# Optimization experiments

Hardware: AMD Instinct MI355X
Metric: run time of the kernel (lower is better)

The kernel has to match this reference:

```python
import jax, jax.numpy as jnp
import numpy as np

B, T, F, H = 1024, 512, 32, 64
EPS = 1e-3  # keras BatchNormalization default epsilon


def lstm_layer(x, Wx, Uh, b):
    """Keras LSTM with activation=relu, recurrent_activation=sigmoid.
    x: [B,T,Fin]; Wx: [Fin,4H]; Uh: [H,4H]; b: [4H]. Gate order i,f,c,o."""
    xz = jnp.einsum('btf,fg->btg', x, Wx) + b  # precompute input projection
    h0 = jnp.zeros((x.shape[0], Uh.shape[0]), x.dtype)

    def step(carry, xz_t):
        h, c = carry
        z = xz_t + h @ Uh
        i, f, g, o = jnp.split(z, 4, axis=-1)
        i = jax.nn.sigmoid(i)
        f = jax.nn.sigmoid(f)
        o = jax.nn.sigmoid(o)
        c = f * c + i * jax.nn.relu(g)
        h = o * jax.nn.relu(c)
        return (h, c), h

    _, hs = jax.lax.scan(step, (h0, h0), jnp.swapaxes(xz, 0, 1))  # [T,B,H]
    return jnp.swapaxes(hs, 0, 1)  # [B,T,H]


def batchnorm(x, gamma, beta, mean, var):
    # inference-mode BN over last axis (keras default axis=-1, training=False)
    return (x - mean) * (gamma * jax.lax.rsqrt(var + EPS)) + beta


def attention(x, W, ht):
    # score = (X @ W) @ h_t -> [B,T]; softmax over time; c_t = X^T @ alpha
    score = jnp.einsum('btd,de,e->bt', x, W, ht[:, 0])
    alpha = jax.nn.softmax(score, axis=1)
    return jnp.einsum('btd,bt->bd', x, alpha)  # [B,H]


def setup_inputs() -> dict:
    key = jax.random.key(0)
    ks = jax.random.split(key, 32)
    d = {'x': jax.random.normal(ks[0], (B, T, F), jnp.float32)}
    fins = [F, H, H]
    for l in range(3):
        fin = fins[l]
        i = l + 1
        d[f'w{i}'] = jax.random.normal(ks[1 + 9 * l], (fin, 4 * H), jnp.float32) * (1.0 / np.sqrt(fin))
        d[f'u{i}'] = jax.random.normal(ks[2 + 9 * l], (H, 4 * H), jnp.float32) * (1.0 / np.sqrt(H))
        d[f'bi{i}'] = jnp.zeros((4 * H,), jnp.float32)
        d[f'gamma{i}'] = jnp.ones((H,), jnp.float32)
        d[f'beta{i}'] = jnp.zeros((H,), jnp.float32)
        d[f'mean{i}'] = jax.random.normal(ks[3 + 9 * l], (H,), jnp.float32) * 0.1
        d[f'var{i}'] = jnp.ones((H,), jnp.float32) + jax.random.uniform(ks[4 + 9 * l], (H,), jnp.float32) * 0.1
        d[f'attw{i}'] = jax.random.truncated_normal(ks[5 + 9 * l], -2, 2, (H, H), jnp.float32) * 0.5
        d[f'attv{i}'] = jax.random.truncated_normal(ks[6 + 9 * l], -2, 2, (H, 1), jnp.float32) * 0.5
    d['dw'] = jax.random.normal(ks[30], (3 * H, 1), jnp.float32) * (1.0 / np.sqrt(3 * H))
    d['db'] = jnp.zeros((1,), jnp.float32)
    return d


def reference(x, w1, u1, bi1, gamma1, beta1, mean1, var1, attw1, attv1,
              w2, u2, bi2, gamma2, beta2, mean2, var2, attw2, attv2,
              w3, u3, bi3, gamma3, beta3, mean3, var3, attw3, attv3,
              dw, db):
    h = lstm_layer(x, w1, u1, bi1)
    h = batchnorm(h, gamma1, beta1, mean1, var1)
    a1 = attention(h, attw1, attv1)
    h = lstm_layer(h, w2, u2, bi2)
    h = batchnorm(h, gamma2, beta2, mean2, var2)
    a2 = attention(h, attw2, attv2)
    h = lstm_layer(h, w3, u3, bi3)
    h = batchnorm(h, gamma3, beta3, mean3, var3)
    a3 = attention(h, attw3, attv3)
    feat = jnp.concatenate([a1, a2, a3], axis=1)  # [B, 3H]
    return feat @ dw + db  # [B, 1]
```

## Files before the change

### kernel.cpp

```cpp
#include <hip/hip_runtime.h>
#include <math.h>

#define BB 1024
#define TT 512
#define FF 32
#define HH 64
#define GG 256
#define TC 64
#define NCHUNK (TT/TC)
#define MB 16
#define NBLK 64
#define HSTR 72
#define EPSBN 1e-3f

typedef __attribute__((ext_vector_type(8))) short bf16x8;
typedef __attribute__((ext_vector_type(4))) float f32x4;
typedef __attribute__((ext_vector_type(4))) int   i32x4;
typedef unsigned short ushort_t;

__global__ void fold1_kernel(const float* __restrict__ gamma, const float* __restrict__ beta,
                             const float* __restrict__ mean, const float* __restrict__ var,
                             const float* __restrict__ attw, const float* __restrict__ attv,
                             float* __restrict__ s_out, float* __restrict__ ab_out,
                             float* __restrict__ wv_out) {
    int d = threadIdx.x;
    float s = gamma[d] * rsqrtf(var[d] + EPSBN);
    float ab = beta[d] - mean[d] * s;
    float wvr = 0.f;
    for (int e = 0; e < HH; ++e) wvr += attw[d * HH + e] * attv[e];
    s_out[d] = s;
    ab_out[d] = ab;
    wv_out[d] = s * wvr;
}

__global__ void fold2_kernel(const float* __restrict__ W, const float* __restrict__ b,
                             const float* __restrict__ s_prev, const float* __restrict__ ab_prev,
                             float* __restrict__ Wp, float* __restrict__ bp) {
    int g = threadIdx.x;
    float bacc = b[g];
    for (int d = 0; d < HH; ++d) {
        float w = W[d * GG + g];
        bacc += ab_prev[d] * w;
        Wp[d * GG + g] = s_prev[d] * w;
    }
    bp[g] = bacc;
}

__global__ void init_kernel(float* st_h, float* st_c, float* st_acc, float* st_m, float* st_d) {
    int i = blockIdx.x * blockDim.x + threadIdx.x;
    int n = 3 * BB * HH;
    if (i < n) { st_h[i] = 0.f; st_c[i] = 0.f; st_acc[i] = 0.f; }
    if (i < 3 * BB) { st_m[i] = -3.0e38f; st_d[i] = 0.f; }
}

__device__ __forceinline__ f32x4 ld4(const float* p) { return *reinterpret_cast<const f32x4*>(p); }
__device__ __forceinline__ void st4(float* p, f32x4 v) { *reinterpret_cast<f32x4*>(p) = v; }
__device__ __forceinline__ bf16x8 ldbf(const ushort_t* p) { return *reinterpret_cast<const bf16x8*>(p); }
__device__ __forceinline__ int cvtpk(float a, float b) {
    int r; asm("v_cvt_pk_bf16_f32 %0, %1, %2" : "=v"(r) : "v"(a), "v"(b)); return r;
}
__device__ __forceinline__ float sigm(float x) { return __fdividef(1.f, 1.f + __expf(-x)); }
#define MFMA(a, b, c) c = __builtin_amdgcn_mfma_f32_16x16x32_bf16(a, b, c, 0, 0, 0)

__global__ void prep_frags(const float* __restrict__ M, int KT, ushort_t* __restrict__ outF) {
    int idx = blockIdx.x * 256 + threadIdx.x;
    int tot = 16 * KT * 512;
    if (idx >= tot) return;
    int e = idx & 7, l = (idx >> 3) & 63, f = idx >> 9;
    int kt = f % KT, gw = f / KT;
    int g = gw & 3, w = gw >> 2;
    int r = l & 15, q = l >> 4;
    int k = 32 * kt + 8 * q + e;
    int col = 64 * g + 16 * w + r;
    float v = M[(size_t)k * GG + col];
    int hb = cvtpk(v, v) & 0xffff;
    float hf = __int_as_float(hb << 16);
    float lo = v - hf;
    int lb = cvtpk(lo, lo) & 0xffff;
    outF[(size_t)(f * 2 + 0) * 512 + l * 8 + e] = (ushort_t)hb;
    outF[(size_t)(f * 2 + 1) * 512 + l * 8 + e] = (ushort_t)lb;
}

__global__ void prep_planes(const float* __restrict__ in, ushort_t* __restrict__ hi,
                            ushort_t* __restrict__ lo, int n4) {
    int i = blockIdx.x * 256 + threadIdx.x;
    if (i >= n4) return;
    f32x4 v = reinterpret_cast<const f32x4*>(in)[i];
    int p0 = cvtpk(v[0], v[1]), p1 = cvtpk(v[2], v[3]);
    float a0 = v[0] - __int_as_float(p0 << 16);
    float a1 = v[1] - __int_as_float(p0 & 0xffff0000);
    float a2 = v[2] - __int_as_float(p1 << 16);
    float a3 = v[3] - __int_as_float(p1 & 0xffff0000);
    int q0 = cvtpk(a0, a1), q1 = cvtpk(a2, a3);
    reinterpret_cast<int2*>(hi)[i] = make_int2(p0, p1);
    reinterpret_cast<int2*>(lo)[i] = make_int2(q0, q1);
}

struct RecFArgs {
    const ushort_t* xhi[3]; const ushort_t* xlo[3]; long sB[3]; long sT[3]; int K[3];
    const ushort_t* UF[3]; const ushort_t* WF[3]; const float* bias[3];
    ushort_t* Hhi[3]; ushort_t* Hlo[3];
    float* st_h[3]; float* st_c[3]; float* st_acc[3];
    float* st_m[3]; float* st_d[3];
    const float* wv[3]; const float* abv[3]; const float* sbn[3];
    float* a_out[3];
    int last[3]; int first[3];
};

template<int KT>
__device__ __forceinline__ void rec_body(const RecFArgs& A, const int seg, const int b0,
                                         ushort_t* hbf, float* scoreP) {
    const int tid = threadIdx.x;
    const int w = tid >> 6;
    const int l = tid & 63;
    const int r = l & 15;
    const int q = l >> 4;
    const int cw = w << 4;
    const int grow = b0 + r;

    const bf16x8* UF = reinterpret_cast<const bf16x8*>(A.UF[seg]);
    const bf16x8* WF = reinterpret_cast<const bf16x8*>(A.WF[seg]);
#define LDU(g,kt,p_) UF[(((((w<<2)+(g))*2+(kt))*2)+(p_))*64 + l]
#define LDW(g,kt,p_) WF[(((((w<<2)+(g))*KT+(kt))*2)+(p_))*64 + l]
    bf16x8 uh00=LDU(0,0,0), uh01=LDU(0,1,0), uh10=LDU(1,0,0), uh11=LDU(1,1,0),
           uh20=LDU(2,0,0), uh21=LDU(2,1,0), uh30=LDU(3,0,0), uh31=LDU(3,1,0);
    bf16x8 ul00=LDU(0,0,1), ul01=LDU(0,1,1), ul10=LDU(1,0,1), ul11=LDU(1,1,1),
           ul20=LDU(2,0,1), ul21=LDU(2,1,1), ul30=LDU(3,0,1), ul31=LDU(3,1,1);
    bf16x8 wh00=LDW(0,0,0), wh10=LDW(1,0,0), wh20=LDW(2,0,0), wh30=LDW(3,0,0);
    bf16x8 wl00=LDW(0,0,1), wl10=LDW(1,0,1), wl20=LDW(2,0,1), wl30=LDW(3,0,1);
    bf16x8 wh01{}, wh11{}, wh21{}, wh31{}, wl01{}, wl11{}, wl21{}, wl31{};
    if constexpr (KT == 2) {
        wh01=LDW(0,1,0); wh11=LDW(1,1,0); wh21=LDW(2,1,0); wh31=LDW(3,1,0);
        wl01=LDW(0,1,1); wl11=LDW(1,1,1); wl21=LDW(2,1,1); wl31=LDW(3,1,1);
    }

    f32x4 bias40 = ld4(A.bias[seg] +   0 + cw + 4 * q);
    f32x4 bias41 = ld4(A.bias[seg] +  64 + cw + 4 * q);
    f32x4 bias42 = ld4(A.bias[seg] + 128 + cw + 4 * q);
    f32x4 bias43 = ld4(A.bias[seg] + 192 + cw + 4 * q);
    f32x4 wv4 = ld4(A.wv[seg] + cw + 4 * q);

    f32x4 c4   = ld4(A.st_c[seg]   + (size_t)grow * HH + cw + 4 * q);
    f32x4 h4   = ld4(A.st_h[seg]   + (size_t)grow * HH + cw + 4 * q);
    f32x4 acc4 = ld4(A.st_acc[seg] + (size_t)grow * HH + cw + 4 * q);
    float m_b = A.st_m[seg][grow];
    float d_b = A.st_d[seg][grow];

    int2 hs_hi, hs_lo;
    auto publish = [&](int slot, f32x4 hv) {
        int p0 = cvtpk(hv[0], hv[1]), p1 = cvtpk(hv[2], hv[3]);
        float a0 = hv[0] - __int_as_float(p0 << 16);
        float a1 = hv[1] - __int_as_float(p0 & 0xffff0000);
        float a2 = hv[2] - __int_as_float(p1 << 16);
        float a3 = hv[3] - __int_as_float(p1 & 0xffff0000);
        int q0 = cvtpk(a0, a1), q1 = cvtpk(a2, a3);
        hs_hi = make_int2(p0, p1); hs_lo = make_int2(q0, q1);
        *reinterpret_cast<int2*>(hbf + ((slot * 2 + 0) * 16 + r) * HSTR + cw + 4 * q) = hs_hi;
        *reinterpret_cast<int2*>(hbf + ((slot * 2 + 1) * 16 + r) * HSTR + cw + 4 * q) = hs_lo;
        float part = hv[0] * wv4[0];
        part = fmaf(hv[1], wv4[1], part);
        part = fmaf(hv[2], wv4[2], part);
        part = fmaf(hv[3], wv4[3], part);
        part += __shfl_xor(part, 16);
        part += __shfl_xor(part, 32);
        if (q == 0) scoreP[(slot * 4 + w) * 16 + r] = part;
    };

    publish(0, h4);

    const ushort_t* xhib = A.xhi[seg] + (size_t)grow * A.sB[seg];
    const ushort_t* xlob = A.xlo[seg] + (size_t)grow * A.sB[seg];
    const long sT = A.sT[seg];

    bf16x8 xh0 = ldbf(xhib + 8 * q), xl0 = ldbf(xlob + 8 * q);
    bf16x8 xh1{}, xl1{};
    if constexpr (KT == 2) { xh1 = ldbf(xhib + 32 + 8 * q); xl1 = ldbf(xlob + 32 + 8 * q); }
    __syncthreads();

    const bool first = A.first[seg] != 0;
    ushort_t* Hhi = A.Hhi[seg];
    ushort_t* Hlo = A.Hlo[seg];

#pragma unroll 2
    for (int t = 0; t < TC; ++t) {
        const int pr = t & 1;
        if (Hhi && t > 0) {
            size_t ho = (size_t)grow * (TC * HH) + (size_t)(t - 1) * HH + cw + 4 * q;
            *reinterpret_cast<int2*>(Hhi + ho) = hs_hi;
            *reinterpret_cast<int2*>(Hlo + ho) = hs_lo;
        }
        float sc = scoreP[(pr * 4 + q) * 16 + r];
        sc += __shfl_xor(sc, 16);
        sc += __shfl_xor(sc, 32);
        if (!(first && t == 0)) {
            float mn = fmaxf(m_b, sc);
            float corr = __expf(m_b - mn);
            float p = __expf(sc - mn);
            d_b = d_b * corr + p;
            acc4 = acc4 * corr + p * h4;
            m_b = mn;
        }
        const int tn = (t + 1 < TC) ? t + 1 : TC - 1;
        const ushort_t* xph = xhib + (size_t)tn * sT + 8 * q;
        const ushort_t* xpl = xlob + (size_t)tn * sT + 8 * q;
        bf16x8 nh0 = ldbf(xph), nl0 = ldbf(xpl), nh1{}, nl1{};
        if constexpr (KT == 2) { nh1 = ldbf(xph + 32); nl1 = ldbf(xpl + 32); }

        const ushort_t* hbh = hbf + (pr * 2 + 0) * 16 * HSTR + r * HSTR;
        const ushort_t* hbl = hbf + (pr * 2 + 1) * 16 * HSTR + r * HSTR;
        bf16x8 bh0 = ldbf(hbh + 8 * q);
        bf16x8 bh1 = ldbf(hbh + 32 + 8 * q);
        bf16x8 bl0 = ldbf(hbl + 8 * q);
        bf16x8 bl1 = ldbf(hbl + 32 + 8 * q);

        f32x4 C0 = bias40;
        MFMA(wh00, xh0, C0); MFMA(wh00, xl0, C0); MFMA(wl00, xh0, C0);
        if constexpr (KT == 2) { MFMA(wh01, xh1, C0); MFMA(wh01, xl1, C0); MFMA(wl01, xh1, C0); }
        MFMA(uh00, bh0, C0); MFMA(uh00, bl0, C0); MFMA(ul00, bh0, C0);
        MFMA(uh01, bh1, C0); MFMA(uh01, bl1, C0); MFMA(ul01, bh1, C0);
        f32x4 C1 = bias41;
        MFMA(wh10, xh0, C1); MFMA(wh10, xl0, C1); MFMA(wl10, xh0, C1);
        if constexpr (KT == 2) { MFMA(wh11, xh1, C1); MFMA(wh11, xl1, C1); MFMA(wl11, xh1, C1); }
        MFMA(uh10, bh0, C1); MFMA(uh10, bl0, C1); MFMA(ul10, bh0, C1);
        MFMA(uh11, bh1, C1); MFMA(uh11, bl1, C1); MFMA(ul11, bh1, C1);
        f32x4 C2 = bias42;
        MFMA(wh20, xh0, C2); MFMA(wh20, xl0, C2); MFMA(wl20, xh0, C2);
        if constexpr (KT == 2) { MFMA(wh21, xh1, C2); MFMA(wh21, xl1, C2); MFMA(wl21, xh1, C2); }
        MFMA(uh20, bh0, C2); MFMA(uh20, bl0, C2); MFMA(ul20, bh0, C2);
        MFMA(uh21, bh1, C2); MFMA(uh21, bl1, C2); MFMA(ul21, bh1, C2);
        f32x4 C3 = bias43;
        MFMA(wh30, xh0, C3); MFMA(wh30, xl0, C3); MFMA(wl30, xh0, C3);
        if constexpr (KT == 2) { MFMA(wh31, xh1, C3); MFMA(wh31, xl1, C3); MFMA(wl31, xh1, C3); }
        MFMA(uh30, bh0, C3); MFMA(uh30, bl0, C3); MFMA(ul30, bh0, C3);
        MFMA(uh31, bh1, C3); MFMA(uh31, bl1, C3); MFMA(ul31, bh1, C3);

#pragma unroll
        for (int i = 0; i < 4; ++i) {
            float zi = sigm(C0[i]);
            float zf = sigm(C1[i]);
            float zg = fmaxf(C2[i], 0.f);
            float zo = sigm(C3[i]);
            c4[i] = fmaf(zf, c4[i], zi * zg);
            h4[i] = zo * fmaxf(c4[i], 0.f);
        }
        publish(pr ^ 1, h4);

        xh0 = nh0; xl0 = nl0;
        if constexpr (KT == 2) { xh1 = nh1; xl1 = nl1; }
        __syncthreads();
    }

    if (Hhi) {
        size_t ho = (size_t)grow * (TC * HH) + (size_t)(TC - 1) * HH + cw + 4 * q;
        *reinterpret_cast<int2*>(Hhi + ho) = hs_hi;
        *reinterpret_cast<int2*>(Hlo + ho) = hs_lo;
    }
    if (A.last[seg]) {
        float sc = scoreP[(0 * 4 + q) * 16 + r];
        sc += __shfl_xor(sc, 16);
        sc += __shfl_xor(sc, 32);
        float mn = fmaxf(m_b, sc);
        float corr = __expf(m_b - mn);
        float p = __expf(sc - mn);
        d_b = d_b * corr + p;
        acc4 = acc4 * corr + p * h4;
        m_b = mn;
        f32x4 sb = ld4(A.sbn[seg] + cw + 4 * q);
        f32x4 ab = ld4(A.abv[seg] + cw + 4 * q);
        f32x4 res;
#pragma unroll
        for (int i = 0; i < 4; ++i)
            res[i] = sb[i] * __fdividef(acc4[i], d_b) + ab[i];
        st4(A.a_out[seg] + (size_t)grow * HH + cw + 4 * q, res);
    }
    st4(A.st_c[seg]   + (size_t)grow * HH + cw + 4 * q, c4);
    st4(A.st_h[seg]   + (size_t)grow * HH + cw + 4 * q, h4);
    st4(A.st_acc[seg] + (size_t)grow * HH + cw + 4 * q, acc4);
    if (w == 0 && q == 0) { A.st_m[seg][grow] = m_b; A.st_d[seg][grow] = d_b; }
#undef LDU
#undef LDW
}

__global__ __launch_bounds__(256, 2) void rec_mfma(RecFArgs A) {
    __shared__ ushort_t hbf[2 * 2 * 16 * HSTR];
    __shared__ float scoreP[2 * 4 * 16];
    const int seg = blockIdx.x >> 6;
    const int b0 = (blockIdx.x & (NBLK - 1)) << 4;
    if (A.K[seg] == 32) rec_body<1>(A, seg, b0, hbf, scoreP);
    else                rec_body<2>(A, seg, b0, hbf, scoreP);
}

__global__ void final_kernel(const float* __restrict__ a, const float* __restrict__ dw,
                             const float* __restrict__ db, float* __restrict__ out) {
    int b = blockIdx.x * blockDim.x + threadIdx.x;
    if (b >= BB) return;
    float acc = db[0];
    for (int l = 0; l < 3; ++l)
        for (int j = 0; j < HH; ++j)
            acc += a[(l * BB + b) * HH + j] * dw[l * HH + j];
    out[b] = acc;
}

extern "C" void kernel_launch(void* const* d_in, const int* in_sizes, int n_in,
                              void* d_out, int out_size, void* d_ws, size_t ws_size,
                              hipStream_t stream) {
    (void)in_sizes; (void)n_in; (void)out_size; (void)ws_size;
    const float* x = (const float*)d_in[0];
    const float* w[3]    = {(const float*)d_in[1],  (const float*)d_in[10], (const float*)d_in[19]};
    const float* uu[3]   = {(const float*)d_in[2],  (const float*)d_in[11], (const float*)d_in[20]};
    const float* bi[3]   = {(const float*)d_in[3],  (const float*)d_in[12], (const float*)d_in[21]};
    const float* gam[3]  = {(const float*)d_in[4],  (const float*)d_in[13], (const float*)d_in[22]};
    const float* bet[3]  = {(const float*)d_in[5],  (const float*)d_in[14], (const float*)d_in[23]};
    const float* mea[3]  = {(const float*)d_in[6],  (const float*)d_in[15], (const float*)d_in[24]};
    const float* var[3]  = {(const float*)d_in[7],  (const float*)d_in[16], (const float*)d_in[25]};
    const float* atw[3]  = {(const float*)d_in[8],  (const float*)d_in[17], (const float*)d_in[26]};
    const float* atv[3]  = {(const float*)d_in[9],  (const float*)d_in[18], (const float*)d_in[27]};
    const float* dw = (const float*)d_in[28];
    const float* db = (const float*)d_in[29];

    float* ws = (float*)d_ws;
    size_t off = 0;
    ushort_t* Hhi[2][2]; ushort_t* Hlo[2][2];
    for (int l = 0; l < 2; ++l)
        for (int p = 0; p < 2; ++p) {
            Hhi[l][p] = (ushort_t*)(ws + off); off += (size_t)BB * TC * HH / 2;
            Hlo[l][p] = (ushort_t*)(ws + off); off += (size_t)BB * TC * HH / 2;
        }
    ushort_t* Xhi = (ushort_t*)(ws + off); off += (size_t)BB * TT * FF / 2;
    ushort_t* Xlo = (ushort_t*)(ws + off); off += (size_t)BB * TT * FF / 2;
    float* st_h  = ws + off; off += 3 * BB * HH;
    float* st_c  = ws + off; off += 3 * BB * HH;
    float* st_ac = ws + off; off += 3 * BB * HH;
    float* st_m  = ws + off; off += 3 * BB;
    float* st_d  = ws + off; off += 3 * BB;
    float* s_ws  = ws + off; off += 3 * HH;
    float* ab_ws = ws + off; off += 3 * HH;
    float* wv_ws = ws + off; off += 3 * HH;
    float* W2p   = ws + off; off += HH * GG;
    float* W3p   = ws + off; off += HH * GG;
    float* b2p   = ws + off; off += GG;
    float* b3p   = ws + off; off += GG;
    float* a_ws  = ws + off; off += 3 * BB * HH;
    ushort_t* UFb[3]; ushort_t* WFb[3];
    for (int l = 0; l < 3; ++l) { UFb[l] = (ushort_t*)(ws + off); off += 16384; }
    for (int l = 0; l < 3; ++l) { WFb[l] = (ushort_t*)(ws + off); off += 16384; }

    for (int l = 0; l < 3; ++l)
        fold1_kernel<<<1, 64, 0, stream>>>(gam[l], bet[l], mea[l], var[l], atw[l], atv[l],
                                           s_ws + l * HH, ab_ws + l * HH, wv_ws + l * HH);
    fold2_kernel<<<1, 256, 0, stream>>>(w[1], bi[1], s_ws + 0 * HH, ab_ws + 0 * HH, W2p, b2p);
    fold2_kernel<<<1, 256, 0, stream>>>(w[2], bi[2], s_ws + 1 * HH, ab_ws + 1 * HH, W3p, b3p);
    init_kernel<<<(3 * BB * HH + 255) / 256, 256, 0, stream>>>(st_h, st_c, st_ac, st_m, st_d);

    for (int l = 0; l < 3; ++l)
        prep_frags<<<64, 256, 0, stream>>>(uu[l], 2, UFb[l]);
    prep_frags<<<32, 256, 0, stream>>>(w[0], 1, WFb[0]);
    prep_frags<<<64, 256, 0, stream>>>(W2p, 2, WFb[1]);
    prep_frags<<<64, 256, 0, stream>>>(W3p, 2, WFb[2]);
    {
        int n4 = BB * TT * FF / 4;
        prep_planes<<<(n4 + 255) / 256, 256, 0, stream>>>(x, Xhi, Xlo, n4);
    }

    const float* bl[3] = {bi[0], b2p, b3p};

    for (int s = 0; s <= NCHUNK - 1 + 2; ++s) {
        RecFArgs ra;
        int nseg = 0;
        for (int l = 0; l < 3; ++l) {
            int cpos = s - l;
            if (cpos < 0 || cpos >= NCHUNK) continue;
            if (l == 0) {
                ra.xhi[nseg] = Xhi + (size_t)cpos * TC * FF;
                ra.xlo[nseg] = Xlo + (size_t)cpos * TC * FF;
                ra.sB[nseg] = (long)TT * FF;
                ra.sT[nseg] = FF;
                ra.K[nseg] = 32;
            } else {
                int par = (s & 1) ^ 1;
                ra.xhi[nseg] = Hhi[l - 1][par];
                ra.xlo[nseg] = Hlo[l - 1][par];
                ra.sB[nseg] = (long)TC * HH;
                ra.sT[nseg] = HH;
                ra.K[nseg] = 64;
            }
            ra.UF[nseg] = UFb[l]; ra.WF[nseg] = WFb[l]; ra.bias[nseg] = bl[l];
            ra.Hhi[nseg] = (l < 2) ? Hhi[l][s & 1] : (ushort_t*)0;
            ra.Hlo[nseg] = (l < 2) ? Hlo[l][s & 1] : (ushort_t*)0;
            ra.st_h[nseg] = st_h + l * BB * HH;
            ra.st_c[nseg] = st_c + l * BB * HH;
            ra.st_acc[nseg] = st_ac + l * BB * HH;
            ra.st_m[nseg] = st_m + l * BB;
            ra.st_d[nseg] = st_d + l * BB;
            ra.wv[nseg]  = wv_ws + l * HH;
            ra.abv[nseg] = ab_ws + l * HH;
            ra.sbn[nseg] = s_ws + l * HH;
            ra.a_out[nseg] = a_ws + l * BB * HH;
            ra.last[nseg]  = (cpos == NCHUNK - 1) ? 1 : 0;
            ra.first[nseg] = (cpos == 0) ? 1 : 0;
            ++nseg;
        }
        if (!nseg) continue;
        rec_mfma<<<nseg * NBLK, 256, 0, stream>>>(ra);
    }
    final_kernel<<<(BB + 255) / 256, 256, 0, stream>>>(a_ws, dw, db, (float*)d_out);
}
```

Baseline: 848.2 us.

## Precompute next step's input projection off the recurrent critical path

The input-projection MFMAs (W·x plus bias) for step t+1 are now computed after the recurrent U·h MFMAs of step t, so only the h-dependent MFMAs sit between barriers. X loads are prefetched two steps ahead with a double-buffered register set. A custom barrier that waits only on LDS counters replaces __syncthreads so outstanding global loads are not drained. Launch bounds drop to one block per CU to make room for the extra registers, which may lower occupancy.

Result: faster. 761.5 us (-10.2%).

```diff
diff --git a/kernel.cpp b/kernel.cpp
--- a/kernel.cpp
+++ b/kernel.cpp
@@ -61,6 +61,12 @@
 }
 __device__ __forceinline__ float sigm(float x) { return __fdividef(1.f, 1.f + __expf(-x)); }
 #define MFMA(a, b, c) c = __builtin_amdgcn_mfma_f32_16x16x32_bf16(a, b, c, 0, 0, 0)
+
+__device__ __forceinline__ void step_barrier() {
+    asm volatile("s_waitcnt lgkmcnt(0)" ::: "memory");
+    __builtin_amdgcn_s_barrier();
+    __builtin_amdgcn_sched_barrier(0);
+}
 
 __global__ void prep_frags(const float* __restrict__ M, int KT, ushort_t* __restrict__ outF) {
     int idx = blockIdx.x * 256 + threadIdx.x;
@@ -172,10 +178,36 @@
     const ushort_t* xlob = A.xlo[seg] + (size_t)grow * A.sB[seg];
     const long sT = A.sT[seg];
 
-    bf16x8 xh0 = ldbf(xhib + 8 * q), xl0 = ldbf(xlob + 8 * q);
-    bf16x8 xh1{}, xl1{};
-    if constexpr (KT == 2) { xh1 = ldbf(xhib + 32 + 8 * q); xl1 = ldbf(xlob + 32 + 8 * q); }
-    __syncthreads();
+    auto xload = [&](int t, bf16x8& h0, bf16x8& l0, bf16x8& h1, bf16x8& l1) {
+        const ushort_t* ph = xhib + (size_t)t * sT + 8 * q;
+        const ushort_t* pl = xlob + (size_t)t * sT + 8 * q;
+        h0 = ldbf(ph); l0 = ldbf(pl);
+        if constexpr (KT == 2) { h1 = ldbf(ph + 32); l1 = ldbf(pl + 32); }
+    };
+
+    f32x4 ZX0, ZX1, ZX2, ZX3;
+    auto buildZX = [&](bf16x8 xh0, bf16x8 xl0, bf16x8 xh1, bf16x8 xl1) {
+        ZX0 = bias40; ZX1 = bias41; ZX2 = bias42; ZX3 = bias43;
+        MFMA(wh00, xh0, ZX0); MFMA(wh00, xl0, ZX0); MFMA(wl00, xh0, ZX0);
+        if constexpr (KT == 2) { MFMA(wh01, xh1, ZX0); MFMA(wh01, xl1, ZX0); MFMA(wl01, xh1, ZX0); }
+        MFMA(wh10, xh0, ZX1); MFMA(wh10, xl0, ZX1); MFMA(wl10, xh0, ZX1);
+        if constexpr (KT == 2) { MFMA(wh11, xh1, ZX1); MFMA(wh11, xl1, ZX1); MFMA(wl11, xh1, ZX1); }
+        MFMA(wh20, xh0, ZX2); MFMA(wh20, xl0, ZX2); MFMA(wl20, xh0, ZX2);
+        if constexpr (KT == 2) { MFMA(wh21, xh1, ZX2); MFMA(wh21, xl1, ZX2); MFMA(wl21, xh1, ZX2); }
+        MFMA(wh30, xh0, ZX3); MFMA(wh30, xl0, ZX3); MFMA(wl30, xh0, ZX3);
+        if constexpr (KT == 2) { MFMA(wh31, xh1, ZX3); MFMA(wh31, xl1, ZX3); MFMA(wl31, xh1, ZX3); }
+    };
+
+    {
+        bf16x8 x0h0, x0l0, x0h1{}, x0l1{};
+        xload(0, x0h0, x0l0, x0h1, x0l1);
+        buildZX(x0h0, x0l0, x0h1, x0l1);
+    }
+    bf16x8 xc_h0, xc_l0, xc_h1{}, xc_l1{};
+    bf16x8 xn_h0, xn_l0, xn_h1{}, xn_l1{};
+    xload(1 < TC ? 1 : TC - 1, xc_h0, xc_l0, xc_h1, xc_l1);
+    xload(2 < TC ? 2 : TC - 1, xn_h0, xn_l0, xn_h1, xn_l1);
+    step_barrier();
 
     const bool first = A.first[seg] != 0;
     ushort_t* Hhi = A.Hhi[seg];
@@ -200,11 +232,6 @@
             acc4 = acc4 * corr + p * h4;
             m_b = mn;
         }
-        const int tn = (t + 1 < TC) ? t + 1 : TC - 1;
-        const ushort_t* xph = xhib + (size_t)tn * sT + 8 * q;
-        const ushort_t* xpl = xlob + (size_t)tn * sT + 8 * q;
-        bf16x8 nh0 = ldbf(xph), nl0 = ldbf(xpl), nh1{}, nl1{};
-        if constexpr (KT == 2) { nh1 = ldbf(xph + 32); nl1 = ldbf(xpl + 32); }
 
         const ushort_t* hbh = hbf + (pr * 2 + 0) * 16 * HSTR + r * HSTR;
         const ushort_t* hbl = hbf + (pr * 2 + 1) * 16 * HSTR + r * HSTR;
@@ -213,26 +240,20 @@
         bf16x8 bl0 = ldbf(hbl + 8 * q);
         bf16x8 bl1 = ldbf(hbl + 32 + 8 * q);
 
-        f32x4 C0 = bias40;
-        MFMA(wh00, xh0, C0); MFMA(wh00, xl0, C0); MFMA(wl00, xh0, C0);
-        if constexpr (KT == 2) { MFMA(wh01, xh1, C0); MFMA(wh01, xl1, C0); MFMA(wl01, xh1, C0); }
+        f32x4 C0 = ZX0, C1 = ZX1, C2 = ZX2, C3 = ZX3;
         MFMA(uh00, bh0, C0); MFMA(uh00, bl0, C0); MFMA(ul00, bh0, C0);
         MFMA(uh01, bh1, C0); MFMA(uh01, bl1, C0); MFMA(ul01, bh1, C0);
-        f32x4 C1 = bias41;
-        MFMA(wh10, xh0, C1); MFMA(wh10, xl0, C1); MFMA(wl10, xh0, C1);
-        if constexpr (KT == 2) { MFMA(wh11, xh1, C1); MFMA(wh11, xl1, C1); MFMA(wl11, xh1, C1); }
         MFMA(uh10, bh0, C1); MFMA(uh10, bl0, C1); MFMA(ul10, bh0, C1);
         MFMA(uh11, bh1, C1); MFMA(uh11, bl1, C1); MFMA(ul11, bh1, C1);
-        f32x4 C2 = bias42;
-        MFMA(wh20, xh0, C2); MFMA(wh20, xl0, C2); MFMA(wl20, xh0, C2);
-        if constexpr (KT == 2) { MFMA(wh21, xh1, C2); MFMA(wh21, xl1, C2); MFMA(wl21, xh1, C2); }
         MFMA(uh20, bh0, C2); MFMA(uh20, bl0, C2); MFMA(ul20, bh0, C2);
         MFMA(uh21, bh1, C2); MFMA(uh21, bl1, C2); MFMA(ul21, bh1, C2);
-        f32x4 C3 = bias43;
-        MFMA(wh30, xh0, C3); MFMA(wh30, xl0, C3); MFMA(wl30, xh0, C3);
-        if constexpr (KT == 2) { MFMA(wh31, xh1, C3); MFMA(wh31, xl1, C3); MFMA(wl31, xh1, C3); }
         MFMA(uh30, bh0, C3); MFMA(uh30, bl0, C3); MFMA(ul30, bh0, C3);
         MFMA(uh31, bh1, C3); MFMA(uh31, bl1, C3); MFMA(ul31, bh1, C3);
+
+        buildZX(xc_h0, xc_l0, xc_h1, xc_l1);
+        xc_h0 = xn_h0; xc_l0 = xn_l0;
+        if constexpr (KT == 2) { xc_h1 = xn_h1; xc_l1 = xn_l1; }
+        { int tn = (t + 3 < TC) ? t + 3 : TC - 1; xload(tn, xn_h0, xn_l0, xn_h1, xn_l1); }
 
 #pragma unroll
         for (int i = 0; i < 4; ++i) {
@@ -244,10 +265,7 @@
             h4[i] = zo * fmaxf(c4[i], 0.f);
         }
         publish(pr ^ 1, h4);
-
-        xh0 = nh0; xl0 = nl0;
-        if constexpr (KT == 2) { xh1 = nh1; xl1 = nl1; }
-        __syncthreads();
+        step_barrier();
     }
 
     if (Hhi) {
@@ -281,7 +299,7 @@
 #undef LDW
 }
 
-__global__ __launch_bounds__(256, 2) void rec_mfma(RecFArgs A) {
+__global__ __launch_bounds__(256, 1) void rec_mfma(RecFArgs A) {
     __shared__ ushort_t hbf[2 * 2 * 16 * HSTR];
     __shared__ float scoreP[2 * 4 * 16];
     const int seg = blockIdx.x >> 6;
```
